# Optimization experiments

Measured on AMD Instinct MI355X. Metric: run time of the kernel, lower is better.

The kernel has to match this reference:

```python
import jax, jax.numpy as jnp
import numpy as np

B, S, D, M = 16, 2048, 1024, 256


def setup_inputs() -> dict:
    key = jax.random.key(0)
    ks = jax.random.split(key, 5)
    w_scale = 0.03  # ~xavier for these fan sizes
    return {
        "x": jax.random.normal(ks[0], (B, S, D), jnp.float32),
        "Wi": jax.random.normal(ks[1], (M, D), jnp.float32) * w_scale,
        "bi": jnp.zeros((M,), jnp.float32),
        "Wf": jax.random.normal(ks[2], (M, D + M), jnp.float32) * w_scale,
        "bf": jnp.ones((M,), jnp.float32),  # forget bias init = 1.0
        "Wu": jax.random.normal(ks[3], (M, D + M), jnp.float32) * w_scale,
        "bu": jnp.zeros((M,), jnp.float32),
        "Wo": jax.random.normal(ks[4], (D, D + M), jnp.float32) * w_scale,
        "bo": jnp.zeros((D,), jnp.float32),
    }


def reference(x, Wi, bi, Wf, bf, Wu, bu, Wo, bo):
    # x: [B, S, D]; gate weights [out, D+M] split into x-part and h-part.
    d = x.shape[-1]
    m = Wi.shape[0]
    WfH, WuH, WoH = Wf[:, d:], Wu[:, d:], Wo[:, d:]
    # Precompute all input-dependent projections (parallel over time).
    xm = jax.nn.silu(jnp.einsum('bsd,md->bsm', x, Wi) + bi)          # SiLU(memory_proj_in(x_t))
    xf = jnp.einsum('bsd,md->bsm', x, Wf[:, :d]) + bf                # x-part of forget gate
    xu = jnp.einsum('bsd,md->bsm', x, Wu[:, :d]) + bu                # x-part of update gate
    xo = x + jnp.einsum('bsd,od->bso', x, Wo[:, :d]) + bo            # residual + x-part of output gate

    def step(h, ts):
        xf_t, xu_t, xm_t, xo_t = ts
        f = jax.nn.sigmoid(xf_t + h @ WfH.T)
        u = jax.nn.sigmoid(xu_t + h @ WuH.T)
        h_new = f * h + u * xm_t            # dropout is identity in eval mode
        out = xo_t + h_new @ WoH.T
        return h_new, out

    h0 = jnp.zeros((x.shape[0], m), x.dtype)
    xs = (xf.swapaxes(0, 1), xu.swapaxes(0, 1), xm.swapaxes(0, 1), xo.swapaxes(0, 1))
    h_final, outs = jax.lax.scan(step, h0, xs)   # outs: [S, B, D]
    return outs.swapaxes(0, 1), h_final
```

## Files before the change

kernel.cpp:

```cpp
#include <hip/hip_runtime.h>
#include <cstdint>
#include <cstddef>

typedef __attribute__((ext_vector_type(8))) short short8;
typedef __attribute__((ext_vector_type(4))) short short4v;
typedef __attribute__((ext_vector_type(4))) float float4v;

typedef __attribute__((address_space(3))) uint32_t lds_u32;
typedef const __attribute__((address_space(1))) uint32_t gl_u32;

__device__ __forceinline__ short f2bf(float f) {
    union { float f; uint32_t u; } v; v.f = f;
    uint32_t r = v.u + 0x7fffu + ((v.u >> 16) & 1u);
    return (short)(r >> 16);
}
__device__ __forceinline__ float bf2f(short s) {
    union { uint32_t u; float f; } v; v.u = ((uint32_t)(uint16_t)s) << 16;
    return v.f;
}
__device__ __forceinline__ float sigmoidf_(float z) {
    return 1.0f / (1.0f + __expf(-z));
}

__global__ __launch_bounds__(256) void xconvert_kernel(const float* __restrict__ x,
                                                       short* __restrict__ Xcat) {
    size_t i = ((size_t)blockIdx.x * 256 + threadIdx.x) * 4;
    size_t r = i >> 10, c = i & 1023;
    float4v v = *(const float4v*)(x + i);
    short4v o;
#pragma unroll
    for (int j = 0; j < 4; ++j) o[j] = f2bf(v[j]);
    *(short4v*)(Xcat + r * 1280 + c) = o;
}

__global__ __launch_bounds__(256) void wconvert_kernel(const float* __restrict__ Wi,
                                                       const float* __restrict__ Wf,
                                                       const float* __restrict__ Wu,
                                                       const float* __restrict__ Wo,
                                                       short* __restrict__ W3b,
                                                       short* __restrict__ Wob) {
    int i = blockIdx.x * 256 + threadIdx.x;
    if (i < 768 * 1024) {
        int n = i >> 10, k = i & 1023;
        const float* src = (n < 256) ? (Wi + (size_t)n * 1024 + k)
                         : (n < 512) ? (Wf + (size_t)(n - 256) * 1280 + k)
                                     : (Wu + (size_t)(n - 512) * 1280 + k);
        W3b[i] = f2bf(*src);
    } else {
        int j = i - 768 * 1024;
        Wob[j] = f2bf(Wo[j]);
    }
}

template <int EPI>
__global__ __launch_bounds__(256) void gemm_bt(const short* __restrict__ A,
                                               const short* __restrict__ Bmat,
                                               const int K, const int lda,
                                               const float* __restrict__ bias1,
                                               const float* __restrict__ bias2,
                                               const float* __restrict__ bias3,
                                               const float* __restrict__ xres,
                                               float* __restrict__ outf,
                                               short* __restrict__ outb) {
    __shared__ __align__(16) short As[4096];
    __shared__ __align__(16) short Bs[4096];

    const int tid = threadIdx.x;
    const int lane = tid & 63;
    const int wv = tid >> 6;
    const int wm = wv >> 1, wn = wv & 1;
    const int row15 = lane & 15;
    const int q = lane >> 4;
    const int tileM = blockIdx.x * 128;
    const int tileN = blockIdx.y * 128;

    float4v acc[4][4];
#pragma unroll
    for (int i = 0; i < 4; ++i)
#pragma unroll
        for (int j = 0; j < 4; ++j) acc[i][j] = {0.f, 0.f, 0.f, 0.f};

    const short* aG = A + (size_t)(tileM + (tid >> 2)) * lda + (tid & 3) * 8;
    const short* bG = Bmat + (size_t)(tileN + (tid >> 2)) * K + (tid & 3) * 8;
    const size_t aStep = (size_t)64 * lda;
    const size_t bStep = (size_t)64 * K;

    lds_u32* AsL = (lds_u32*)As;
    lds_u32* BsL = (lds_u32*)Bs;
    const int base1 = wv * 256;
    const int base2 = 1024 + wv * 256;

    for (int kt = 0; kt < K; kt += 32) {
        __builtin_amdgcn_global_load_lds((gl_u32*)aG,           AsL + base1, 16, 0, 0);
        __builtin_amdgcn_global_load_lds((gl_u32*)(aG + aStep), AsL + base2, 16, 0, 0);
        __builtin_amdgcn_global_load_lds((gl_u32*)bG,           BsL + base1, 16, 0, 0);
        __builtin_amdgcn_global_load_lds((gl_u32*)(bG + bStep), BsL + base2, 16, 0, 0);
        aG += 32; bG += 32;
        __syncthreads();

        short8 af[4], bf8[4];
#pragma unroll
        for (int mt = 0; mt < 4; ++mt)
            af[mt] = *(const short8*)(As + (wm * 64 + mt * 16 + row15) * 32 + q * 8);
#pragma unroll
        for (int nt = 0; nt < 4; ++nt)
            bf8[nt] = *(const short8*)(Bs + (wn * 64 + nt * 16 + row15) * 32 + q * 8);
#pragma unroll
        for (int mt = 0; mt < 4; ++mt)
#pragma unroll
            for (int nt = 0; nt < 4; ++nt)
                acc[mt][nt] = __builtin_amdgcn_mfma_f32_16x16x32_bf16(af[mt], bf8[nt], acc[mt][nt], 0, 0, 0);
        __syncthreads();
    }

#pragma unroll
    for (int mt = 0; mt < 4; ++mt) {
#pragma unroll
        for (int nt = 0; nt < 4; ++nt) {
#pragma unroll
            for (int r = 0; r < 4; ++r) {
                const int gr = tileM + wm * 64 + mt * 16 + q * 4 + r;
                const int gc = tileN + wn * 64 + nt * 16 + row15;
                float v = acc[mt][nt][r];
                if (EPI == 1) {
                    float bias = (gc < 256) ? bias1[gc] : (gc < 512) ? bias2[gc - 256] : bias3[gc - 512];
                    float z = v + bias;
                    if (gc < 256) z = z * sigmoidf_(z);
                    outb[(size_t)gr * 768 + gc] = f2bf(z);
                } else {
                    const size_t idx = (size_t)gr * 1024 + gc;
                    outf[idx] = v + bias1[gc] + xres[idx];
                }
            }
        }
    }
}

__global__ __launch_bounds__(512) void scan_kernel(const float* __restrict__ Wfp,
                                                   const float* __restrict__ Wup,
                                                   const short* __restrict__ xmfu,
                                                   short* __restrict__ Xcat,
                                                   float* __restrict__ hfinal) {
    __shared__ __align__(16) short hb[4096];
    __shared__ __align__(16) short xstage[2][6144];
    __shared__ __align__(16) float fuz[512];

    const int tid = threadIdx.x;
    const int lane = tid & 63;
    const int w = tid >> 6;
    const int sel = w >> 2;
    const int n0 = (w & 3) * 64;
    const int row15 = lane & 15;
    const int q = lane >> 4;
    const int b = blockIdx.x;

    const short* xm_b = xmfu + (size_t)b * 1572864;

    for (int i = tid; i < 4096; i += 512) hb[i] = 0;

    const float* WH = sel ? Wup : Wfp;
    short8 bfrag[8][4];
#pragma unroll
    for (int ks = 0; ks < 8; ++ks)
#pragma unroll
        for (int nt = 0; nt < 4; ++nt) {
            const float* src = WH + (size_t)(n0 + nt * 16 + row15) * 1280 + 1024 + ks * 32 + q * 8;
            float4v v0 = *(const float4v*)(src);
            float4v v1 = *(const float4v*)(src + 4);
            short8 v;
#pragma unroll
            for (int j = 0; j < 4; ++j) { v[j] = f2bf(v0[j]); v[j + 4] = f2bf(v1[j]); }
            bfrag[ks][nt] = v;
        }

    const bool isLoader = (tid >= 256);
    const int lw = (tid - 256) >> 6;
    lds_u32* xl = (lds_u32*)(&xstage[0][0]);

    if (isLoader) {
#pragma unroll
        for (int i = 0; i < 3; ++i)
            __builtin_amdgcn_global_load_lds((gl_u32*)(xm_b + i * 2048 + lw * 512 + lane * 8),
                                             xl + (i * 1024 + lw * 256), 16, 0, 0);
        __builtin_amdgcn_sched_barrier(0);
        asm volatile("s_waitcnt vmcnt(0)" ::: "memory");
        __builtin_amdgcn_sched_barrier(0);
    }
    __builtin_amdgcn_sched_barrier(0);
    asm volatile("s_waitcnt lgkmcnt(0)" ::: "memory");
    __builtin_amdgcn_sched_barrier(0);
    __builtin_amdgcn_s_barrier();
    __builtin_amdgcn_sched_barrier(0);

    float hreg = 0.f;
    const int m = tid;
    const int mks = m >> 5, mq = (m >> 3) & 3, mj = m & 7;
    const int hslot = mks * 512 + (mq * 18 + mks) * 8 + mj;
    short* Xout = Xcat + (size_t)b * 2048 * 1280 + 1024 + m;

    short8 afr = {0, 0, 0, 0, 0, 0, 0, 0};

#pragma unroll 1
    for (int j = 0; j < 256; ++j) {
        const int buf = j & 1;
        if (isLoader && (j + 1 < 256)) {
            const short* src = xm_b + (size_t)(j + 1) * 6144;
#pragma unroll
            for (int i = 0; i < 3; ++i)
                __builtin_amdgcn_global_load_lds((gl_u32*)(src + i * 2048 + lw * 512 + lane * 8),
                                                 xl + ((buf ^ 1) * 3072 + i * 1024 + lw * 256), 16, 0, 0);
        }
        const short* xs = &xstage[buf][0];
#pragma unroll
        for (int s = 0; s < 8; ++s) {
            float4v a0 = {0.f, 0.f, 0.f, 0.f}, a1 = {0.f, 0.f, 0.f, 0.f};
            float4v a2 = {0.f, 0.f, 0.f, 0.f}, a3 = {0.f, 0.f, 0.f, 0.f};
#pragma unroll
            for (int ks = 0; ks < 8; ++ks) {
                if (row15 == 0)
                    afr = *(const short8*)(hb + ks * 512 + (q * 18 + ks) * 8);
                a0 = __builtin_amdgcn_mfma_f32_16x16x32_bf16(afr, bfrag[ks][0], a0, 0, 0, 0);
                a1 = __builtin_amdgcn_mfma_f32_16x16x32_bf16(afr, bfrag[ks][1], a1, 0, 0, 0);
                a2 = __builtin_amdgcn_mfma_f32_16x16x32_bf16(afr, bfrag[ks][2], a2, 0, 0, 0);
                a3 = __builtin_amdgcn_mfma_f32_16x16x32_bf16(afr, bfrag[ks][3], a3, 0, 0, 0);
            }
            if (lane < 16) {
                float4v v = {a0[0], a1[0], a2[0], a3[0]};
                *(float4v*)(fuz + sel * 256 + (w & 3) * 64 + lane * 4) = v;
            }
            __builtin_amdgcn_sched_barrier(0);
            asm volatile("s_waitcnt lgkmcnt(0)" ::: "memory");
            __builtin_amdgcn_sched_barrier(0);
            __builtin_amdgcn_s_barrier();
            __builtin_amdgcn_sched_barrier(0);
            if (tid < 256) {
                const int fidx = (m >> 6) * 64 + (m & 15) * 4 + ((m >> 4) & 3);
                const float zf = fuz[fidx];
                const float zu = fuz[256 + fidx];
                const float zbf = bf2f(xs[s * 768 + 256 + m]);
                const float zbu = bf2f(xs[s * 768 + 512 + m]);
                const float xmv = bf2f(xs[s * 768 + m]);
                const float f = sigmoidf_(zf + zbf);
                const float u = sigmoidf_(zu + zbu);
                const float hn = f * hreg + u * xmv;
                hreg = hn;
                const short hnb = f2bf(hn);
                hb[hslot] = hnb;
                Xout[(size_t)(j * 8 + s) * 1280] = hnb;
            }
            if (s == 7 && isLoader) {
                __builtin_amdgcn_sched_barrier(0);
                asm volatile("s_waitcnt vmcnt(0)" ::: "memory");
                __builtin_amdgcn_sched_barrier(0);
            }
            __builtin_amdgcn_sched_barrier(0);
            asm volatile("s_waitcnt lgkmcnt(0)" ::: "memory");
            __builtin_amdgcn_sched_barrier(0);
            __builtin_amdgcn_s_barrier();
            __builtin_amdgcn_sched_barrier(0);
        }
    }
    if (tid < 256) hfinal[b * 256 + m] = hreg;
}

extern "C" void kernel_launch(void* const* d_in, const int* in_sizes, int n_in,
                              void* d_out, int out_size, void* d_ws, size_t ws_size,
                              hipStream_t stream) {
    const float* x  = (const float*)d_in[0];
    const float* Wi = (const float*)d_in[1];
    const float* bi = (const float*)d_in[2];
    const float* Wf = (const float*)d_in[3];
    const float* bf = (const float*)d_in[4];
    const float* Wu = (const float*)d_in[5];
    const float* bu = (const float*)d_in[6];
    const float* Wo = (const float*)d_in[7];
    const float* bo = (const float*)d_in[8];
    float* out = (float*)d_out;

    char* ws = (char*)d_ws;
    short* Xcat = (short*)ws;
    short* xmfu = (short*)(ws + 83886080ULL);
    short* W3b  = (short*)(ws + 83886080ULL + 50331648ULL);
    short* Wob  = (short*)(ws + 83886080ULL + 50331648ULL + 1572864ULL);

    xconvert_kernel<<<dim3(32768), dim3(256), 0, stream>>>(x, Xcat);
    wconvert_kernel<<<dim3(8192), dim3(256), 0, stream>>>(Wi, Wf, Wu, Wo, W3b, Wob);
    gemm_bt<1><<<dim3(256, 6), dim3(256), 0, stream>>>(Xcat, W3b, 1024, 1280,
                                                       bi, bf, bu, nullptr, nullptr, xmfu);
    scan_kernel<<<dim3(16), dim3(512), 0, stream>>>(Wf, Wu, xmfu, Xcat, out + 33554432);
    gemm_bt<2><<<dim3(256, 8), dim3(256), 0, stream>>>(Xcat, Wob, 1280, 1280,
                                                       bo, nullptr, nullptr, x, out, nullptr);
}
```

Baseline: 2.219 ms.

## Compute both gates per wave to remove one barrier per scan step

Each wave now owns 32 hidden units and computes both the forget and update gate MFMAs for them. Lanes 0-15 apply the gate math and the h update directly from accumulator registers, with h double-buffered in LDS. This removes the fuz LDS exchange and one of the two block barriers per timestep in the serial recurrence. In exchange each wave holds more B fragments in registers, only 16 lanes per wave do the elementwise work, and the launch bounds now request two blocks per CU.

```diff
diff --git a/kernel.cpp b/kernel.cpp
--- a/kernel.cpp
+++ b/kernel.cpp
@@ -136,42 +136,42 @@
     }
 }
 
-__global__ __launch_bounds__(512) void scan_kernel(const float* __restrict__ Wfp,
-                                                   const float* __restrict__ Wup,
-                                                   const short* __restrict__ xmfu,
-                                                   short* __restrict__ Xcat,
-                                                   float* __restrict__ hfinal) {
-    __shared__ __align__(16) short hb[4096];
+__global__ __launch_bounds__(512, 2) void scan_kernel(const float* __restrict__ Wfp,
+                                                      const float* __restrict__ Wup,
+                                                      const short* __restrict__ xmfu,
+                                                      short* __restrict__ Xcat,
+                                                      float* __restrict__ hfinal) {
+    __shared__ __align__(16) short hb[2][256];
     __shared__ __align__(16) short xstage[2][6144];
-    __shared__ __align__(16) float fuz[512];
 
     const int tid = threadIdx.x;
     const int lane = tid & 63;
     const int w = tid >> 6;
-    const int sel = w >> 2;
-    const int n0 = (w & 3) * 64;
+    const int n0 = w * 32;
     const int row15 = lane & 15;
     const int q = lane >> 4;
     const int b = blockIdx.x;
 
     const short* xm_b = xmfu + (size_t)b * 1572864;
 
-    for (int i = tid; i < 4096; i += 512) hb[i] = 0;
-
-    const float* WH = sel ? Wup : Wfp;
-    short8 bfrag[8][4];
+    ((short*)hb)[tid] = 0;
+
+    short8 bfrag[8][2][2];
 #pragma unroll
     for (int ks = 0; ks < 8; ++ks)
 #pragma unroll
-        for (int nt = 0; nt < 4; ++nt) {
-            const float* src = WH + (size_t)(n0 + nt * 16 + row15) * 1280 + 1024 + ks * 32 + q * 8;
-            float4v v0 = *(const float4v*)(src);
-            float4v v1 = *(const float4v*)(src + 4);
-            short8 v;
-#pragma unroll
-            for (int j = 0; j < 4; ++j) { v[j] = f2bf(v0[j]); v[j + 4] = f2bf(v1[j]); }
-            bfrag[ks][nt] = v;
-        }
+        for (int sel = 0; sel < 2; ++sel)
+#pragma unroll
+            for (int nt = 0; nt < 2; ++nt) {
+                const float* WH = sel ? Wup : Wfp;
+                const float* src = WH + (size_t)(n0 + nt * 16 + row15) * 1280 + 1024 + ks * 32 + q * 8;
+                float4v v0 = *(const float4v*)(src);
+                float4v v1 = *(const float4v*)(src + 4);
+                short8 v;
+#pragma unroll
+                for (int j = 0; j < 4; ++j) { v[j] = f2bf(v0[j]); v[j + 4] = f2bf(v1[j]); }
+                bfrag[ks][sel][nt] = v;
+            }
 
     const bool isLoader = (tid >= 256);
     const int lw = (tid - 256) >> 6;
@@ -192,11 +192,10 @@
     __builtin_amdgcn_s_barrier();
     __builtin_amdgcn_sched_barrier(0);
 
-    float hreg = 0.f;
-    const int m = tid;
-    const int mks = m >> 5, mq = (m >> 3) & 3, mj = m & 7;
-    const int hslot = mks * 512 + (mq * 18 + mks) * 8 + mj;
-    short* Xout = Xcat + (size_t)b * 2048 * 1280 + 1024 + m;
+    float h1 = 0.f, h2 = 0.f;
+    const int m1 = n0 + row15;
+    short* Xout1 = Xcat + (size_t)b * 2048 * 1280 + 1024 + m1;
+    short* Xout2 = Xout1 + 16;
 
     short8 afr = {0, 0, 0, 0, 0, 0, 0, 0};
 
@@ -213,40 +212,40 @@
         const short* xs = &xstage[buf][0];
 #pragma unroll
         for (int s = 0; s < 8; ++s) {
-            float4v a0 = {0.f, 0.f, 0.f, 0.f}, a1 = {0.f, 0.f, 0.f, 0.f};
-            float4v a2 = {0.f, 0.f, 0.f, 0.f}, a3 = {0.f, 0.f, 0.f, 0.f};
+            const int p = s & 1;
+            float xmv1, xmv2, zf1, zf2, zu1, zu2;
+            if (lane < 16) {
+                xmv1 = bf2f(xs[s * 768 + m1]);
+                zf1  = bf2f(xs[s * 768 + 256 + m1]);
+                zu1  = bf2f(xs[s * 768 + 512 + m1]);
+                xmv2 = bf2f(xs[s * 768 + 16 + m1]);
+                zf2  = bf2f(xs[s * 768 + 272 + m1]);
+                zu2  = bf2f(xs[s * 768 + 528 + m1]);
+            }
+            float4v af0 = {0.f, 0.f, 0.f, 0.f}, af1 = {0.f, 0.f, 0.f, 0.f};
+            float4v au0 = {0.f, 0.f, 0.f, 0.f}, au1 = {0.f, 0.f, 0.f, 0.f};
 #pragma unroll
             for (int ks = 0; ks < 8; ++ks) {
                 if (row15 == 0)
-                    afr = *(const short8*)(hb + ks * 512 + (q * 18 + ks) * 8);
-                a0 = __builtin_amdgcn_mfma_f32_16x16x32_bf16(afr, bfrag[ks][0], a0, 0, 0, 0);
-                a1 = __builtin_amdgcn_mfma_f32_16x16x32_bf16(afr, bfrag[ks][1], a1, 0, 0, 0);
-                a2 = __builtin_amdgcn_mfma_f32_16x16x32_bf16(afr, bfrag[ks][2], a2, 0, 0, 0);
-                a3 = __builtin_amdgcn_mfma_f32_16x16x32_bf16(afr, bfrag[ks][3], a3, 0, 0, 0);
+                    afr = *(const short8*)(&hb[p][ks * 32 + q * 8]);
+                af0 = __builtin_amdgcn_mfma_f32_16x16x32_bf16(afr, bfrag[ks][0][0], af0, 0, 0, 0);
+                af1 = __builtin_amdgcn_mfma_f32_16x16x32_bf16(afr, bfrag[ks][0][1], af1, 0, 0, 0);
+                au0 = __builtin_amdgcn_mfma_f32_16x16x32_bf16(afr, bfrag[ks][1][0], au0, 0, 0, 0);
+                au1 = __builtin_amdgcn_mfma_f32_16x16x32_bf16(afr, bfrag[ks][1][1], au1, 0, 0, 0);
             }
             if (lane < 16) {
-                float4v v = {a0[0], a1[0], a2[0], a3[0]};
-                *(float4v*)(fuz + sel * 256 + (w & 3) * 64 + lane * 4) = v;
-            }
-            __builtin_amdgcn_sched_barrier(0);
-            asm volatile("s_waitcnt lgkmcnt(0)" ::: "memory");
-            __builtin_amdgcn_sched_barrier(0);
-            __builtin_amdgcn_s_barrier();
-            __builtin_amdgcn_sched_barrier(0);
-            if (tid < 256) {
-                const int fidx = (m >> 6) * 64 + (m & 15) * 4 + ((m >> 4) & 3);
-                const float zf = fuz[fidx];
-                const float zu = fuz[256 + fidx];
-                const float zbf = bf2f(xs[s * 768 + 256 + m]);
-                const float zbu = bf2f(xs[s * 768 + 512 + m]);
-                const float xmv = bf2f(xs[s * 768 + m]);
-                const float f = sigmoidf_(zf + zbf);
-                const float u = sigmoidf_(zu + zbu);
-                const float hn = f * hreg + u * xmv;
-                hreg = hn;
-                const short hnb = f2bf(hn);
-                hb[hslot] = hnb;
-                Xout[(size_t)(j * 8 + s) * 1280] = hnb;
+                const float f1 = sigmoidf_(af0[0] + zf1);
+                const float u1 = sigmoidf_(au0[0] + zu1);
+                const float f2 = sigmoidf_(af1[0] + zf2);
+                const float u2 = sigmoidf_(au1[0] + zu2);
+                h1 = f1 * h1 + u1 * xmv1;
+                h2 = f2 * h2 + u2 * xmv2;
+                const short s1 = f2bf(h1), s2 = f2bf(h2);
+                hb[p ^ 1][m1] = s1;
+                hb[p ^ 1][m1 + 16] = s2;
+                const size_t off = (size_t)(j * 8 + s) * 1280;
+                Xout1[off] = s1;
+                Xout2[off] = s2;
             }
             if (s == 7 && isLoader) {
                 __builtin_amdgcn_sched_barrier(0);
@@ -260,7 +259,10 @@
             __builtin_amdgcn_sched_barrier(0);
         }
     }
-    if (tid < 256) hfinal[b * 256 + m] = hreg;
+    if (lane < 16) {
+        hfinal[b * 256 + m1] = h1;
+        hfinal[b * 256 + m1 + 16] = h2;
+    }
 }
 
 extern "C" void kernel_launch(void* const* d_in, const int* in_sizes, int n_in,
```

Result: slower. 2.417 ms (+8.9%).
